# Performance work log

Measured on AMD Instinct MI355X. Metric: run time of the kernel, lower is better.

## Reference

```python
import jax, jax.numpy as jnp
import numpy as np

U = 200000      # unique nodes
B = 20000       # node_list batch size
K = 33          # n_nbr_samples + self
F = 256         # feature_dim
E = 128         # emb_dim
BN_EPS = 1e-5


def setup_inputs() -> dict:
    key = jax.random.key(0)
    k1, k2, k3, k4 = jax.random.split(key, 4)
    return {
        "features": jax.random.normal(k1, (U, F), dtype=jnp.float32),
        "W": jax.random.normal(k2, (F, E), dtype=jnp.float32) * 0.05,
        "b": jax.random.normal(k3, (E,), dtype=jnp.float32) * 0.01,
        "gamma": jnp.ones((E,), dtype=jnp.float32),
        "beta": jnp.zeros((E,), dtype=jnp.float32),
        "sample_idx": jax.random.randint(k4, (B, K), 0, U, dtype=jnp.int64)
        if jax.config.jax_enable_x64 else jax.random.randint(k4, (B, K), 0, U, dtype=jnp.int32),
    }


def reference(features, W, b, gamma, beta, sample_idx):
    # fc: Linear -> BatchNorm1d (training-mode batch stats) -> Tanh; Dropout in eval (identity)
    h = features @ W + b                       # [U, E]
    mu = jnp.mean(h, axis=0)                   # [E]
    var = jnp.var(h, axis=0)                   # biased var, as torch BN uses for normalization
    h = jnp.tanh(gamma * (h - mu) * jax.lax.rsqrt(var + BN_EPS) + beta)  # [U, E]
    # Row-normalized 0/1 mask matmul == mean over the K distinct sampled unique-node rows
    gathered = h[sample_idx]                   # [B, K, E] irregular gather
    return jnp.mean(gathered, axis=1)          # [B, E]
```

## Files before the change

### kernel.cpp

```cpp
#include <hip/hip_runtime.h>

#define U_NODES 200000
#define B_ROWS  20000
#define K_S     33
#define F_DIM   256
#define E_DIM   128
#define NPART   128

typedef __bf16 bf16x8 __attribute__((ext_vector_type(8)));
typedef float  f32x4  __attribute__((ext_vector_type(4)));
typedef unsigned short ushortx8 __attribute__((ext_vector_type(8)));

__device__ __forceinline__ unsigned short f2bf(float f) {
    unsigned int u = __builtin_bit_cast(unsigned int, f);
    u += 0x7fffu + ((u >> 16) & 1u);
    return (unsigned short)(u >> 16);
}
__device__ __forceinline__ float bf2f(unsigned short s) {
    return __builtin_bit_cast(float, ((unsigned int)s) << 16);
}

__global__ void wprep_kernel(const float* __restrict__ W, unsigned short* __restrict__ Wt) {
    int n = blockIdx.x;
    int k = threadIdx.x;
    Wt[n * F_DIM + k] = f2bf(W[(size_t)k * E_DIM + n]);
}

__global__ __launch_bounds__(256) void gemm_stats_kernel(
    const float* __restrict__ A, const unsigned short* __restrict__ Wt,
    unsigned short* __restrict__ h, float* __restrict__ part)
{
    __shared__ __attribute__((aligned(16))) char smem[32768];

    const int t    = threadIdx.x;
    const int lane = t & 63;
    const int wv   = t >> 6;
    const int m    = lane & 15;
    const int qd   = lane >> 4;
    const int row0 = blockIdx.x * 128;

    const int r0 = row0 + wv * 32 + m;
    const int r1 = r0 + 16;
    const float* A0 = A + (size_t)min(r0, U_NODES - 1) * F_DIM + qd * 8;
    const float* A1 = A + (size_t)min(r1, U_NODES - 1) * F_DIM + qd * 8;

    f32x4 acc0[8], acc1[8];
    #pragma unroll
    for (int ct = 0; ct < 8; ++ct) {
        acc0[ct] = (f32x4){0.f, 0.f, 0.f, 0.f};
        acc1[ct] = (f32x4){0.f, 0.f, 0.f, 0.f};
    }

    #pragma unroll
    for (int half = 0; half < 2; ++half) {
        if (half) __syncthreads();
        #pragma unroll
        for (int i = 0; i < 8; ++i) {
            int of = t + 256 * i;
            int n = of >> 4, o = of & 15;
            ushortx8 v = *(const ushortx8*)(Wt + n * F_DIM + half * 128 + o * 8);
            *(ushortx8*)(smem + n * 256 + (((o & 8) | ((o ^ n) & 7)) << 4)) = v;
        }
        __syncthreads();
        #pragma unroll
        for (int kf = 0; kf < 4; ++kf) {
            const float* a0p = A0 + half * 128 + kf * 32;
            const float* a1p = A1 + half * 128 + kf * 32;
            float a0f[8], a1f[8];
            *(float4*)&a0f[0] = *(const float4*)(a0p);
            *(float4*)&a0f[4] = *(const float4*)(a0p + 4);
            *(float4*)&a1f[0] = *(const float4*)(a1p);
            *(float4*)&a1f[4] = *(const float4*)(a1p + 4);
            ushortx8 u0, u1;
            #pragma unroll
            for (int j = 0; j < 8; ++j) { u0[j] = f2bf(a0f[j]); u1[j] = f2bf(a1f[j]); }
            bf16x8 a0 = __builtin_bit_cast(bf16x8, u0);
            bf16x8 a1 = __builtin_bit_cast(bf16x8, u1);
            int o = kf * 4 + qd;
            #pragma unroll
            for (int ct = 0; ct < 8; ++ct) {
                int n = ct * 16 + m;
                bf16x8 b = *(const bf16x8*)(smem + n * 256 + (((o & 8) | ((o ^ n) & 7)) << 4));
                acc0[ct] = __builtin_amdgcn_mfma_f32_16x16x32_bf16(a0, b, acc0[ct], 0, 0, 0);
                acc1[ct] = __builtin_amdgcn_mfma_f32_16x16x32_bf16(a1, b, acc1[ct], 0, 0, 0);
            }
        }
    }
    __syncthreads();

    const bool full = (row0 + 128) <= U_NODES;
    float s[8], sq[8];
    #pragma unroll
    for (int ct = 0; ct < 8; ++ct) {
        float ss = 0.f, qq = 0.f;
        #pragma unroll
        for (int v = 0; v < 4; ++v) {
            float x0 = acc0[ct][v];
            float x1 = acc1[ct][v];
            if (full || (row0 + wv * 32 + qd * 4 + v) < U_NODES)      { ss += x0; qq += x0 * x0; }
            if (full || (row0 + wv * 32 + 16 + qd * 4 + v) < U_NODES) { ss += x1; qq += x1 * x1; }
        }
        s[ct] = ss; sq[ct] = qq;
    }
    float* red = (float*)smem;
    int rq = wv * 4 + qd;
    #pragma unroll
    for (int ct = 0; ct < 8; ++ct) {
        red[rq * 256 + ct * 16 + m]       = s[ct];
        red[rq * 256 + 128 + ct * 16 + m] = sq[ct];
    }
    __syncthreads();
    {
        float tot = 0.f;
        #pragma unroll
        for (int i = 0; i < 16; ++i) tot += red[i * 256 + t];
        atomicAdd(&part[(blockIdx.x & (NPART - 1)) * 256 + t], tot);
    }
    __syncthreads();

    unsigned short* tb = (unsigned short*)(smem + wv * 8192);
    #pragma unroll
    for (int ct = 0; ct < 8; ++ct)
        #pragma unroll
        for (int v = 0; v < 4; ++v) {
            tb[(qd * 4 + v) * 128 + ct * 16 + m]      = f2bf(acc0[ct][v]);
            tb[(16 + qd * 4 + v) * 128 + ct * 16 + m] = f2bf(acc1[ct][v]);
        }
    __syncthreads();
    #pragma unroll
    for (int i = 0; i < 8; ++i) {
        int idx = lane + 64 * i;
        int r = idx >> 4, c8 = (idx & 15) * 8;
        int gr = row0 + wv * 32 + r;
        if (gr < U_NODES)
            *(ushortx8*)(h + (size_t)gr * E_DIM + c8) = *(const ushortx8*)(tb + r * 128 + c8);
    }
}

__global__ void finalize_kernel(const float* __restrict__ part,
                                const float* __restrict__ gamma, const float* __restrict__ beta,
                                float* __restrict__ scale, float* __restrict__ shift)
{
    int e = threadIdx.x;
    float sum = 0.f, sq = 0.f;
    for (int p = 0; p < NPART; ++p) {
        sum += part[p * 256 + e];
        sq  += part[p * 256 + 128 + e];
    }
    float mu  = sum * (1.f / U_NODES);
    float var = sq * (1.f / U_NODES) - mu * mu;
    float inv = rsqrtf(var + 1e-5f);
    float sc  = gamma[e] * inv;
    scale[e] = sc;
    shift[e] = beta[e] - sc * mu;
}

__global__ __launch_bounds__(256, 4) void gather_kernel(
    const unsigned short* __restrict__ h, const int* __restrict__ sidx_g,
    const float* __restrict__ scale, const float* __restrict__ shift,
    float* __restrict__ out)
{
    __shared__ int sl[16 * K_S];
    const int t  = threadIdx.x;
    const int g  = t & 15;
    const int r  = t >> 4;
    const int b0 = blockIdx.x * 16;
    for (int i = t; i < 16 * K_S; i += 256) sl[i] = sidx_g[(size_t)b0 * K_S + i];
    float scv[8], shv[8];
    *(float4*)&scv[0] = *(const float4*)(scale + g * 8);
    *(float4*)&scv[4] = *(const float4*)(scale + g * 8 + 4);
    *(float4*)&shv[0] = *(const float4*)(shift + g * 8);
    *(float4*)&shv[4] = *(const float4*)(shift + g * 8 + 4);
    __syncthreads();

    float acc[8] = {0.f, 0.f, 0.f, 0.f, 0.f, 0.f, 0.f, 0.f};
    #pragma unroll
    for (int k = 0; k < K_S; ++k) {
        int idx = sl[r * K_S + k];
        ushortx8 v = *(const ushortx8*)(h + (size_t)idx * E_DIM + g * 8);
        #pragma unroll
        for (int j = 0; j < 8; ++j) {
            float x = bf2f(v[j]) * scv[j] + shv[j];
            acc[j] += 1.f - 2.f * __builtin_amdgcn_rcpf(__expf(2.f * x) + 1.f);
        }
    }
    float* op = out + (size_t)(b0 + r) * E_DIM + g * 8;
    *(float4*)(op)     = make_float4(acc[0] * (1.f / K_S), acc[1] * (1.f / K_S),
                                     acc[2] * (1.f / K_S), acc[3] * (1.f / K_S));
    *(float4*)(op + 4) = make_float4(acc[4] * (1.f / K_S), acc[5] * (1.f / K_S),
                                     acc[6] * (1.f / K_S), acc[7] * (1.f / K_S));
}

extern "C" void kernel_launch(void* const* d_in, const int* in_sizes, int n_in,
                              void* d_out, int out_size, void* d_ws, size_t ws_size,
                              hipStream_t stream) {
    const float* features = (const float*)d_in[0];
    const float* W        = (const float*)d_in[1];
    const float* gamma    = (const float*)d_in[3];
    const float* beta     = (const float*)d_in[4];
    const int*   sample   = (const int*)d_in[5];
    float* out = (float*)d_out;

    float* part  = (float*)d_ws;
    float* scale = part + NPART * 256;
    float* shift = scale + 128;
    unsigned short* Wt = (unsigned short*)(shift + 128);
    unsigned short* h  = Wt + 128 * 256;

    hipMemsetAsync(part, 0, NPART * 256 * sizeof(float), stream);
    wprep_kernel<<<128, 256, 0, stream>>>(W, Wt);
    gemm_stats_kernel<<<(U_NODES + 127) / 128, 256, 0, stream>>>(features, Wt, h, part);
    finalize_kernel<<<1, 128, 0, stream>>>(part, gamma, beta, scale, shift);
    gather_kernel<<<B_ROWS / 16, 256, 0, stream>>>(h, sample, scale, shift, out);
}
```

Before: 355.4 us.

## Restructure GEMM to 64-row tiles with upfront A loads, and narrow the gather per thread

The GEMM kernel now handles 64 rows per block with one row tile per wave. Each thread issues all of its A-row loads up front, before staging W, and prefetches the second half of W into registers while the first-half MFMAs run. Launch bounds ask for 4 blocks per CU to raise occupancy and hide the memory latency of streaming the features matrix. The gather kernel now processes 8 batch rows per block, with each thread loading 4 bf16 values (8 bytes) instead of 16. This doubles the thread count, giving more parallel outstanding gathers at the cost of narrower loads.

```diff
diff --git a/kernel.cpp b/kernel.cpp
--- a/kernel.cpp
+++ b/kernel.cpp
@@ -26,7 +26,7 @@
     Wt[n * F_DIM + k] = f2bf(W[(size_t)k * E_DIM + n]);
 }
 
-__global__ __launch_bounds__(256) void gemm_stats_kernel(
+__global__ __launch_bounds__(256, 4) void gemm_stats_kernel(
     const float* __restrict__ A, const unsigned short* __restrict__ Wt,
     unsigned short* __restrict__ h, float* __restrict__ part)
 {
@@ -37,77 +37,82 @@
     const int wv   = t >> 6;
     const int m    = lane & 15;
     const int qd   = lane >> 4;
-    const int row0 = blockIdx.x * 128;
-
-    const int r0 = row0 + wv * 32 + m;
-    const int r1 = r0 + 16;
-    const float* A0 = A + (size_t)min(r0, U_NODES - 1) * F_DIM + qd * 8;
-    const float* A1 = A + (size_t)min(r1, U_NODES - 1) * F_DIM + qd * 8;
-
-    f32x4 acc0[8], acc1[8];
-    #pragma unroll
-    for (int ct = 0; ct < 8; ++ct) {
-        acc0[ct] = (f32x4){0.f, 0.f, 0.f, 0.f};
-        acc1[ct] = (f32x4){0.f, 0.f, 0.f, 0.f};
-    }
-
-    #pragma unroll
-    for (int half = 0; half < 2; ++half) {
-        if (half) __syncthreads();
-        #pragma unroll
-        for (int i = 0; i < 8; ++i) {
-            int of = t + 256 * i;
-            int n = of >> 4, o = of & 15;
-            ushortx8 v = *(const ushortx8*)(Wt + n * F_DIM + half * 128 + o * 8);
-            *(ushortx8*)(smem + n * 256 + (((o & 8) | ((o ^ n) & 7)) << 4)) = v;
+    const int row0 = blockIdx.x * 64;
+    const int row  = row0 + wv * 16 + m;
+
+    const float* Ap = A + (size_t)row * F_DIM + qd * 8;
+    float a[8][8];
+    #pragma unroll
+    for (int kf = 0; kf < 8; ++kf) {
+        *(float4*)&a[kf][0] = *(const float4*)(Ap + kf * 32);
+        *(float4*)&a[kf][4] = *(const float4*)(Ap + kf * 32 + 4);
+    }
+
+    #pragma unroll
+    for (int i = 0; i < 8; ++i) {
+        int of = t + 256 * i, n = of >> 4, o = of & 15;
+        ushortx8 v = *(const ushortx8*)(Wt + n * F_DIM + o * 8);
+        *(ushortx8*)(smem + n * 256 + (((o & 8) | ((o ^ n) & 7)) << 4)) = v;
+    }
+
+    bf16x8 af[8];
+    #pragma unroll
+    for (int kf = 0; kf < 8; ++kf) {
+        ushortx8 u;
+        #pragma unroll
+        for (int j = 0; j < 8; ++j) u[j] = f2bf(a[kf][j]);
+        af[kf] = __builtin_bit_cast(bf16x8, u);
+    }
+
+    f32x4 acc[8];
+    #pragma unroll
+    for (int ct = 0; ct < 8; ++ct) acc[ct] = (f32x4){0.f, 0.f, 0.f, 0.f};
+
+    __syncthreads();
+    #pragma unroll
+    for (int kfl = 0; kfl < 4; ++kfl) {
+        int o = kfl * 4 + qd;
+        #pragma unroll
+        for (int ct = 0; ct < 8; ++ct) {
+            int n = ct * 16 + m;
+            bf16x8 b = *(const bf16x8*)(smem + n * 256 + (((o & 8) | ((o ^ n) & 7)) << 4));
+            acc[ct] = __builtin_amdgcn_mfma_f32_16x16x32_bf16(af[kfl], b, acc[ct], 0, 0, 0);
         }
-        __syncthreads();
-        #pragma unroll
-        for (int kf = 0; kf < 4; ++kf) {
-            const float* a0p = A0 + half * 128 + kf * 32;
-            const float* a1p = A1 + half * 128 + kf * 32;
-            float a0f[8], a1f[8];
-            *(float4*)&a0f[0] = *(const float4*)(a0p);
-            *(float4*)&a0f[4] = *(const float4*)(a0p + 4);
-            *(float4*)&a1f[0] = *(const float4*)(a1p);
-            *(float4*)&a1f[4] = *(const float4*)(a1p + 4);
-            ushortx8 u0, u1;
-            #pragma unroll
-            for (int j = 0; j < 8; ++j) { u0[j] = f2bf(a0f[j]); u1[j] = f2bf(a1f[j]); }
-            bf16x8 a0 = __builtin_bit_cast(bf16x8, u0);
-            bf16x8 a1 = __builtin_bit_cast(bf16x8, u1);
-            int o = kf * 4 + qd;
-            #pragma unroll
-            for (int ct = 0; ct < 8; ++ct) {
-                int n = ct * 16 + m;
-                bf16x8 b = *(const bf16x8*)(smem + n * 256 + (((o & 8) | ((o ^ n) & 7)) << 4));
-                acc0[ct] = __builtin_amdgcn_mfma_f32_16x16x32_bf16(a0, b, acc0[ct], 0, 0, 0);
-                acc1[ct] = __builtin_amdgcn_mfma_f32_16x16x32_bf16(a1, b, acc1[ct], 0, 0, 0);
-            }
+    }
+    ushortx8 wreg[8];
+    #pragma unroll
+    for (int i = 0; i < 8; ++i) {
+        int of = t + 256 * i, n = of >> 4, o = of & 15;
+        wreg[i] = *(const ushortx8*)(Wt + n * F_DIM + 128 + o * 8);
+    }
+    __syncthreads();
+    #pragma unroll
+    for (int i = 0; i < 8; ++i) {
+        int of = t + 256 * i, n = of >> 4, o = of & 15;
+        *(ushortx8*)(smem + n * 256 + (((o & 8) | ((o ^ n) & 7)) << 4)) = wreg[i];
+    }
+    __syncthreads();
+    #pragma unroll
+    for (int kfl = 0; kfl < 4; ++kfl) {
+        int o = kfl * 4 + qd;
+        #pragma unroll
+        for (int ct = 0; ct < 8; ++ct) {
+            int n = ct * 16 + m;
+            bf16x8 b = *(const bf16x8*)(smem + n * 256 + (((o & 8) | ((o ^ n) & 7)) << 4));
+            acc[ct] = __builtin_amdgcn_mfma_f32_16x16x32_bf16(af[4 + kfl], b, acc[ct], 0, 0, 0);
         }
     }
     __syncthreads();
 
-    const bool full = (row0 + 128) <= U_NODES;
-    float s[8], sq[8];
+    float* red = (float*)smem;
+    int rq = wv * 4 + qd;
     #pragma unroll
     for (int ct = 0; ct < 8; ++ct) {
         float ss = 0.f, qq = 0.f;
         #pragma unroll
-        for (int v = 0; v < 4; ++v) {
-            float x0 = acc0[ct][v];
-            float x1 = acc1[ct][v];
-            if (full || (row0 + wv * 32 + qd * 4 + v) < U_NODES)      { ss += x0; qq += x0 * x0; }
-            if (full || (row0 + wv * 32 + 16 + qd * 4 + v) < U_NODES) { ss += x1; qq += x1 * x1; }
-        }
-        s[ct] = ss; sq[ct] = qq;
-    }
-    float* red = (float*)smem;
-    int rq = wv * 4 + qd;
-    #pragma unroll
-    for (int ct = 0; ct < 8; ++ct) {
-        red[rq * 256 + ct * 16 + m]       = s[ct];
-        red[rq * 256 + 128 + ct * 16 + m] = sq[ct];
+        for (int v = 0; v < 4; ++v) { float x = acc[ct][v]; ss += x; qq += x * x; }
+        red[rq * 256 + ct * 16 + m]       = ss;
+        red[rq * 256 + 128 + ct * 16 + m] = qq;
     }
     __syncthreads();
     {
@@ -118,22 +123,19 @@
     }
     __syncthreads();
 
-    unsigned short* tb = (unsigned short*)(smem + wv * 8192);
+    unsigned short* tb = (unsigned short*)(smem + wv * 4096);
     #pragma unroll
     for (int ct = 0; ct < 8; ++ct)
         #pragma unroll
-        for (int v = 0; v < 4; ++v) {
-            tb[(qd * 4 + v) * 128 + ct * 16 + m]      = f2bf(acc0[ct][v]);
-            tb[(16 + qd * 4 + v) * 128 + ct * 16 + m] = f2bf(acc1[ct][v]);
-        }
-    __syncthreads();
-    #pragma unroll
-    for (int i = 0; i < 8; ++i) {
+        for (int v = 0; v < 4; ++v)
+            tb[(qd * 4 + v) * 128 + ct * 16 + m] = f2bf(acc[ct][v]);
+    __syncthreads();
+    #pragma unroll
+    for (int i = 0; i < 4; ++i) {
         int idx = lane + 64 * i;
         int r = idx >> 4, c8 = (idx & 15) * 8;
-        int gr = row0 + wv * 32 + r;
-        if (gr < U_NODES)
-            *(ushortx8*)(h + (size_t)gr * E_DIM + c8) = *(const ushortx8*)(tb + r * 128 + c8);
+        int gr = row0 + wv * 16 + r;
+        *(ushortx8*)(h + (size_t)gr * E_DIM + c8) = *(const ushortx8*)(tb + r * 128 + c8);
     }
 }
 
@@ -160,35 +162,36 @@
     const float* __restrict__ scale, const float* __restrict__ shift,
     float* __restrict__ out)
 {
-    __shared__ int sl[16 * K_S];
-    const int t  = threadIdx.x;
-    const int g  = t & 15;
-    const int r  = t >> 4;
-    const int b0 = blockIdx.x * 16;
-    for (int i = t; i < 16 * K_S; i += 256) sl[i] = sidx_g[(size_t)b0 * K_S + i];
-    float scv[8], shv[8];
-    *(float4*)&scv[0] = *(const float4*)(scale + g * 8);
-    *(float4*)&scv[4] = *(const float4*)(scale + g * 8 + 4);
-    *(float4*)&shv[0] = *(const float4*)(shift + g * 8);
-    *(float4*)&shv[4] = *(const float4*)(shift + g * 8 + 4);
-    __syncthreads();
-
-    float acc[8] = {0.f, 0.f, 0.f, 0.f, 0.f, 0.f, 0.f, 0.f};
+    __shared__ int sl[8 * K_S];
+    const int t    = threadIdx.x;
+    const int lane = t & 63;
+    const int wv   = t >> 6;
+    const int sub  = lane >> 5;
+    const int e    = lane & 31;
+    const int rloc = wv * 2 + sub;
+    const int b0   = blockIdx.x * 8;
+    for (int i = t; i < 8 * K_S; i += 256) sl[i] = sidx_g[(size_t)b0 * K_S + i];
+    float scv[4], shv[4];
+    *(float4*)scv = *(const float4*)(scale + e * 4);
+    *(float4*)shv = *(const float4*)(shift + e * 4);
+    __syncthreads();
+
+    float acc[4] = {0.f, 0.f, 0.f, 0.f};
     #pragma unroll
     for (int k = 0; k < K_S; ++k) {
-        int idx = sl[r * K_S + k];
-        ushortx8 v = *(const ushortx8*)(h + (size_t)idx * E_DIM + g * 8);
-        #pragma unroll
-        for (int j = 0; j < 8; ++j) {
-            float x = bf2f(v[j]) * scv[j] + shv[j];
+        int idx = sl[rloc * K_S + k];
+        uint2 v = *(const uint2*)(h + (size_t)idx * E_DIM + e * 4);
+        unsigned short c[4] = { (unsigned short)(v.x & 0xffff), (unsigned short)(v.x >> 16),
+                                (unsigned short)(v.y & 0xffff), (unsigned short)(v.y >> 16) };
+        #pragma unroll
+        for (int j = 0; j < 4; ++j) {
+            float x = bf2f(c[j]) * scv[j] + shv[j];
             acc[j] += 1.f - 2.f * __builtin_amdgcn_rcpf(__expf(2.f * x) + 1.f);
         }
     }
-    float* op = out + (size_t)(b0 + r) * E_DIM + g * 8;
-    *(float4*)(op)     = make_float4(acc[0] * (1.f / K_S), acc[1] * (1.f / K_S),
-                                     acc[2] * (1.f / K_S), acc[3] * (1.f / K_S));
-    *(float4*)(op + 4) = make_float4(acc[4] * (1.f / K_S), acc[5] * (1.f / K_S),
-                                     acc[6] * (1.f / K_S), acc[7] * (1.f / K_S));
+    *(float4*)(out + (size_t)(b0 + rloc) * E_DIM + e * 4) =
+        make_float4(acc[0] * (1.f / K_S), acc[1] * (1.f / K_S),
+                    acc[2] * (1.f / K_S), acc[3] * (1.f / K_S));
 }
 
 extern "C" void kernel_launch(void* const* d_in, const int* in_sizes, int n_in,
@@ -209,7 +212,7 @@
 
     hipMemsetAsync(part, 0, NPART * 256 * sizeof(float), stream);
     wprep_kernel<<<128, 256, 0, stream>>>(W, Wt);
-    gemm_stats_kernel<<<(U_NODES + 127) / 128, 256, 0, stream>>>(features, Wt, h, part);
+    gemm_stats_kernel<<<U_NODES / 64, 256, 0, stream>>>(features, Wt, h, part);
     finalize_kernel<<<1, 128, 0, stream>>>(part, gamma, beta, scale, shift);
-    gather_kernel<<<B_ROWS / 16, 256, 0, stream>>>(h, sample, scale, shift, out);
-}
+    gather_kernel<<<B_ROWS / 8, 256, 0, stream>>>(h, sample, scale, shift, out);
+}
```

Measured after the change: 350.7 us. Within noise of the previous version (-1.3%).
